# Performance work log

Hardware: AMD Instinct MI355X
Metric: run time of the kernel (lower is better)

The kernel has to match this reference:

```python
import jax, jax.numpy as jnp
import numpy as np

DPW = 1.0       # dist_push_weight
IW = 1.0        # intensity_weight
MINDIST = 0.05
MAXVAL = 255.0
KS = 11         # gaussian blur kernel size


def _gaussian_blur(img):
    """torchvision-style gaussian_blur with kernel_size=11, default sigma, reflect pad. img: [B,H,W]."""
    sigma = 0.3 * ((KS - 1) * 0.5 - 1) + 0.8  # = 2.0
    half = (KS - 1) * 0.5
    x = jnp.linspace(-half, half, KS)
    pdf = jnp.exp(-0.5 * (x / sigma) ** 2)
    k1 = (pdf / pdf.sum()).astype(img.dtype)
    pad = KS // 2
    xp = jnp.pad(img, ((0, 0), (pad, pad), (pad, pad)), mode='reflect')
    lhs = xp[:, None]  # [B,1,H+2p,W+2p]
    kh = k1.reshape(1, 1, KS, 1)
    kw = k1.reshape(1, 1, 1, KS)
    y = jax.lax.conv_general_dilated(lhs, kh, (1, 1), 'VALID')
    y = jax.lax.conv_general_dilated(y, kw, (1, 1), 'VALID')
    return y[:, 0]


def _dist_push(tr):
    """tr: [N,2]. mean over upper-triangle pairs of clamp(mindist - dist, 0)."""
    n = tr.shape[0]
    sq = jnp.sum(tr * tr, axis=-1)                       # [N]
    d2 = sq[:, None] + sq[None, :] - 2.0 * (tr @ tr.T)   # [N,N]
    d2 = jnp.maximum(d2, 0.0)
    mask = jnp.triu(jnp.ones((n, n), dtype=bool), k=1)
    d = jnp.sqrt(jnp.where(mask, d2, 1.0))               # safe sqrt off-mask
    vals = jnp.where(mask, jnp.maximum(MINDIST - d, 0.0), 0.0)
    npairs = n * (n - 1) // 2
    return jnp.sum(vals) / npairs


def _intensity(x, trace):
    """x: [H,W] blurred image, trace: [N,2] in [0,1]. Returns per-point bilinear-ish intensity [N]."""
    H, W = x.shape
    idx0 = trace[:, 0] * H
    idx1 = trace[:, 1] * W
    xp = jnp.pad(x, ((0, 2), (0, 2)), mode='reflect')    # reflect pad right/bottom by 2
    i0 = jax.lax.stop_gradient(jnp.floor(idx0 + 0.5))
    i1 = i0 + 1.0
    j0 = jax.lax.stop_gradient(jnp.floor(idx1 + 0.5))
    j1 = j0 + 1.0
    i0i = i0.astype(jnp.int32); i1i = i1.astype(jnp.int32)
    j0i = j0.astype(jnp.int32); j1i = j1.astype(jnp.int32)
    y00 = xp[i0i, j0i]
    y10 = xp[i1i, j0i]
    y01 = xp[i0i, j1i]
    out_ax0 = (i1 - idx0) * y00 + (idx0 - i0) * y10
    out_ax1 = (j1 - idx1) * y00 + (idx1 - j0) * y01
    return (out_ax0 + out_ax1) / 2.0


def setup_inputs() -> dict:
    key = jax.random.key(0)
    k1, k2 = jax.random.split(key)
    trace = jax.random.uniform(k1, (8, 4096, 2), dtype=jnp.float32)
    img = jax.random.uniform(k2, (8, 512, 512), dtype=jnp.float32)
    return {"trace": trace, "img": img}


def reference(trace, img):
    dist_push_loss = jnp.mean(jax.vmap(_dist_push)(trace))
    imgf = _gaussian_blur(img)
    intensity = jax.vmap(_intensity)(imgf, trace)   # [B,N]
    int_loss = jnp.mean(MAXVAL - intensity)
    return dist_push_loss * DPW + int_loss * IW
```

## Files before the change

kernel.cpp:

```cpp
#include <hip/hip_runtime.h>

#define IMW 512
#define NP 4096

#define GATHER_BLOCKS 128
#define DIST_BLOCKS 1024
#define TOTAL_BLOCKS (GATHER_BLOCKS + DIST_BLOCKS)

__device__ constexpr float KW[11] = {
    0.00881223f, 0.02714359f, 0.06511407f, 0.12164908f, 0.17699836f,
    0.20056542f, 0.17699836f, 0.12164908f, 0.06511407f, 0.02714359f, 0.00881223f};

__device__ __forceinline__ int refl(int r) {
    r = r < 0 ? -r : r;
    return r > 511 ? 1022 - r : r;
}

__global__ __launch_bounds__(256)
void fused_compute(const float* __restrict__ trace, const float* __restrict__ img,
                   float* __restrict__ partials) {
    const int tid = threadIdx.x;
    const int bx = blockIdx.x;
    __shared__ float2 pj[512];
    __shared__ float red[4];
    float local;

    if (bx < GATHER_BLOCKS) {
        const int b = bx >> 4;
        const int p = (bx & 15) * 256 + tid;
        const float2 t2 = ((const float2*)trace)[b * NP + p];
        const float idx0 = t2.x * 512.f, idx1 = t2.y * 512.f;
        const float i0f = floorf(idx0 + 0.5f), j0f = floorf(idx1 + 0.5f);
        const float wi = idx0 - i0f, wj = idx1 - j0f;
        const int i0 = (int)i0f, j0 = (int)j0f;
        const int mi0 = refl(i0), mi1 = refl(i0 + 1);
        const int mj0 = refl(j0), mj1 = refl(j0 + 1);
        const int ilo = min(mi0, mi1), jlo = min(mj0, mj1);
        const bool sr = mi0 > mi1, sc = mj0 > mj1;
        const float* srcb = img + b * (IMW * IMW);

        float v0[12], v1[12];
        int R[12];
#pragma unroll
        for (int a = 0; a < 12; ++a) R[a] = refl(ilo - 5 + a) * IMW;
#pragma unroll
        for (int c = 0; c < 12; ++c) {
            const int cc = refl(jlo - 5 + c);
            const float* col = srcb + cc;
            float lo = 0.f, hi = 0.f;
#pragma unroll
            for (int a = 0; a < 12; ++a) {
                const float pv = col[R[a]];
                if (a < 11) lo = fmaf(KW[a], pv, lo);
                if (a > 0) hi = fmaf(KW[a - 1], pv, hi);
            }
            v0[c] = sr ? hi : lo;
            v1[c] = sr ? lo : hi;
        }
        float y00lo = 0.f, y00hi = 0.f, y10lo = 0.f, y10hi = 0.f;
#pragma unroll
        for (int c = 0; c < 11; ++c) {
            y00lo = fmaf(KW[c], v0[c], y00lo);
            y00hi = fmaf(KW[c], v0[c + 1], y00hi);
            y10lo = fmaf(KW[c], v1[c], y10lo);
            y10hi = fmaf(KW[c], v1[c + 1], y10hi);
        }
        const float y00 = sc ? y00hi : y00lo;
        const float y01 = sc ? y00lo : y00hi;
        const float y10 = sc ? y10hi : y10lo;
        local = 0.5f * ((1.f - wi) * y00 + wi * y10 + (1.f - wj) * y00 + wj * y01);
    } else {
        const int d = bx - GATHER_BLOCKS;
        const int b = d >> 7, ib = (d >> 3) & 15, jc = d & 7;
        const float2* tb = (const float2*)(trace + b * NP * 2);
        const float2 pi = tb[ib * 256 + tid];
        pj[tid] = tb[jc * 512 + tid];
        pj[tid + 256] = tb[jc * 512 + tid + 256];
        __syncthreads();
        float s = 0.f;
#pragma unroll 8
        for (int j = 0; j < 512; ++j) {
            const float dx = pi.x - pj[j].x;
            const float dy = pi.y - pj[j].y;
            const float d2 = fmaf(dx, dx, dy * dy);
            s += fminf(__builtin_amdgcn_sqrtf(d2), 0.05f);
        }
        local = s;
    }

    for (int o = 32; o; o >>= 1) local += __shfl_down(local, o, 64);
    if ((tid & 63) == 0) red[tid >> 6] = local;
    __syncthreads();
    if (tid == 0) partials[bx] = red[0] + red[1] + red[2] + red[3];
}

__global__ __launch_bounds__(256)
void finalize(const float* __restrict__ partials, float* __restrict__ out) {
    const int tid = threadIdx.x;
    float sg = 0.f, sd = 0.f;
    for (int i = tid; i < TOTAL_BLOCKS; i += 256) {
        const float v = partials[i];
        if (i < GATHER_BLOCKS) sg += v; else sd += v;
    }
    for (int o = 32; o; o >>= 1) {
        sg += __shfl_down(sg, o, 64);
        sd += __shfl_down(sd, o, 64);
    }
    __shared__ float rg[4], rd[4];
    if ((tid & 63) == 0) { rg[tid >> 6] = sg; rd[tid >> 6] = sd; }
    __syncthreads();
    if (tid == 0) {
        const double M  = (double)(rd[0] + rd[1] + rd[2] + rd[3]);
        const double S1 = (double)(rg[0] + rg[1] + rg[2] + rg[3]);
        const double dp = (6709248.0 - M) / 134184960.0;
        const double il = 255.0 - S1 / 32768.0;
        out[0] = (float)(dp + il);
    }
}

extern "C" void kernel_launch(void* const* d_in, const int* in_sizes, int n_in,
                              void* d_out, int out_size, void* d_ws, size_t ws_size,
                              hipStream_t stream) {
    const float* trace = (const float*)d_in[0];
    const float* img = (const float*)d_in[1];
    float* partials = (float*)d_ws;
    float* out = (float*)d_out;

    fused_compute<<<TOTAL_BLOCKS, 256, 0, stream>>>(trace, img, partials);
    finalize<<<1, 256, 0, stream>>>(partials, out);
}
```

Baseline: 106.6 us.

## Replace all-pairs distance loop with per-batch uniform grid neighbor search

The pairwise dist-push term is now computed with a 20x20 uniform grid: each of 8 blocks bins its batch's 4096 points by counting sort in shared memory, then each point only tests the points in its 3x3 neighbouring cells against the 0.05 cutoff. This removes the O(N^2) dense distance evaluation. The gather path switches to row-major separable blur order, and both paths now use 1024-thread blocks, which cuts the grid from 1152 blocks to 40. The risks are low parallelism on a large GPU (only 8 distance blocks), serial prefix scans and atomics, and divergent per-thread loop lengths.

```diff
diff --git a/kernel.cpp b/kernel.cpp
--- a/kernel.cpp
+++ b/kernel.cpp
@@ -2,10 +2,14 @@
 
 #define IMW 512
 #define NP 4096
+#define NB 8
 
-#define GATHER_BLOCKS 128
-#define DIST_BLOCKS 1024
+#define GATHER_BLOCKS 32
+#define DIST_BLOCKS 8
 #define TOTAL_BLOCKS (GATHER_BLOCKS + DIST_BLOCKS)
+
+#define NCELL 20
+#define NCELL2 400
 
 __device__ constexpr float KW[11] = {
     0.00881223f, 0.02714359f, 0.06511407f, 0.12164908f, 0.17699836f,
@@ -16,19 +20,23 @@
     return r > 511 ? 1022 - r : r;
 }
 
-__global__ __launch_bounds__(256)
+__global__ __launch_bounds__(1024)
 void fused_compute(const float* __restrict__ trace, const float* __restrict__ img,
                    float* __restrict__ partials) {
     const int tid = threadIdx.x;
     const int bx = blockIdx.x;
-    __shared__ float2 pj[512];
-    __shared__ float red[4];
+    __shared__ float2 sorted[NP];
+    __shared__ int cellcnt[NCELL2];
+    __shared__ int cellstart[NCELL2];
+    __shared__ int cursor[NCELL2];
+    __shared__ int offs[512];
+    __shared__ float red[16];
     float local;
 
     if (bx < GATHER_BLOCKS) {
-        const int b = bx >> 4;
-        const int p = (bx & 15) * 256 + tid;
-        const float2 t2 = ((const float2*)trace)[b * NP + p];
+        const int p = bx * 1024 + tid;
+        const int b = p >> 12;
+        const float2 t2 = ((const float2*)trace)[b * NP + (p & (NP - 1))];
         const float idx0 = t2.x * 512.f, idx1 = t2.y * 512.f;
         const float i0f = floorf(idx0 + 0.5f), j0f = floorf(idx1 + 0.5f);
         const float wi = idx0 - i0f, wj = idx1 - j0f;
@@ -39,51 +47,91 @@
         const bool sr = mi0 > mi1, sc = mj0 > mj1;
         const float* srcb = img + b * (IMW * IMW);
 
-        float v0[12], v1[12];
-        int R[12];
+        int cc[12], R[12];
 #pragma unroll
-        for (int a = 0; a < 12; ++a) R[a] = refl(ilo - 5 + a) * IMW;
+        for (int c = 0; c < 12; ++c) cc[c] = refl(jlo - 5 + c);
 #pragma unroll
-        for (int c = 0; c < 12; ++c) {
-            const int cc = refl(jlo - 5 + c);
-            const float* col = srcb + cc;
+        for (int r = 0; r < 12; ++r) R[r] = refl(ilo - 5 + r) * IMW;
+
+        float A_lo = 0.f, A_hi = 0.f, B_lo = 0.f, B_hi = 0.f;
+#pragma unroll
+        for (int r = 0; r < 12; ++r) {
+            const float* base = srcb + R[r];
             float lo = 0.f, hi = 0.f;
 #pragma unroll
-            for (int a = 0; a < 12; ++a) {
-                const float pv = col[R[a]];
-                if (a < 11) lo = fmaf(KW[a], pv, lo);
-                if (a > 0) hi = fmaf(KW[a - 1], pv, hi);
+            for (int c = 0; c < 12; ++c) {
+                const float v = base[cc[c]];
+                if (c < 11) lo = fmaf(KW[c], v, lo);
+                if (c > 0) hi = fmaf(KW[c - 1], v, hi);
             }
-            v0[c] = sr ? hi : lo;
-            v1[c] = sr ? lo : hi;
+            if (r < 11) { A_lo = fmaf(KW[r], lo, A_lo); B_lo = fmaf(KW[r], hi, B_lo); }
+            if (r > 0)  { A_hi = fmaf(KW[r - 1], lo, A_hi); B_hi = fmaf(KW[r - 1], hi, B_hi); }
         }
-        float y00lo = 0.f, y00hi = 0.f, y10lo = 0.f, y10hi = 0.f;
-#pragma unroll
-        for (int c = 0; c < 11; ++c) {
-            y00lo = fmaf(KW[c], v0[c], y00lo);
-            y00hi = fmaf(KW[c], v0[c + 1], y00hi);
-            y10lo = fmaf(KW[c], v1[c], y10lo);
-            y10hi = fmaf(KW[c], v1[c + 1], y10hi);
-        }
-        const float y00 = sc ? y00hi : y00lo;
-        const float y01 = sc ? y00lo : y00hi;
-        const float y10 = sc ? y10hi : y10lo;
+        const float yA  = sr ? A_hi : A_lo;
+        const float yA1 = sr ? A_lo : A_hi;
+        const float yB  = sr ? B_hi : B_lo;
+        const float yB1 = sr ? B_lo : B_hi;
+        const float y00 = sc ? yB : yA;
+        const float y01 = sc ? yA : yB;
+        const float y10 = sc ? yB1 : yA1;
         local = 0.5f * ((1.f - wi) * y00 + wi * y10 + (1.f - wj) * y00 + wj * y01);
     } else {
-        const int d = bx - GATHER_BLOCKS;
-        const int b = d >> 7, ib = (d >> 3) & 15, jc = d & 7;
+        const int b = bx - GATHER_BLOCKS;
         const float2* tb = (const float2*)(trace + b * NP * 2);
-        const float2 pi = tb[ib * 256 + tid];
-        pj[tid] = tb[jc * 512 + tid];
-        pj[tid + 256] = tb[jc * 512 + tid + 256];
+        float2 r4[4];
+        int c4[4];
+#pragma unroll
+        for (int k = 0; k < 4; ++k) {
+            const float2 pt = tb[tid + 1024 * k];
+            r4[k] = pt;
+            const int cx = min((int)(pt.x * 20.f), NCELL - 1);
+            const int cy = min((int)(pt.y * 20.f), NCELL - 1);
+            c4[k] = cy * NCELL + cx;
+        }
+        if (tid < NCELL2) cellcnt[tid] = 0;
+        __syncthreads();
+#pragma unroll
+        for (int k = 0; k < 4; ++k) atomicAdd(&cellcnt[c4[k]], 1);
+        __syncthreads();
+        if (tid < 512) offs[tid] = (tid < NCELL2) ? cellcnt[tid] : 0;
+        __syncthreads();
+        for (int s = 1; s < 512; s <<= 1) {
+            int v = 0;
+            if (tid < 512 && tid >= s) v = offs[tid - s];
+            __syncthreads();
+            if (tid < 512) offs[tid] += v;
+            __syncthreads();
+        }
+        if (tid < NCELL2) {
+            const int st = offs[tid] - cellcnt[tid];
+            cellstart[tid] = st;
+            cursor[tid] = st;
+        }
+        __syncthreads();
+#pragma unroll
+        for (int k = 0; k < 4; ++k) {
+            const int pos = atomicAdd(&cursor[c4[k]], 1);
+            sorted[pos] = r4[k];
+        }
         __syncthreads();
         float s = 0.f;
-#pragma unroll 8
-        for (int j = 0; j < 512; ++j) {
-            const float dx = pi.x - pj[j].x;
-            const float dy = pi.y - pj[j].y;
-            const float d2 = fmaf(dx, dx, dy * dy);
-            s += fminf(__builtin_amdgcn_sqrtf(d2), 0.05f);
+#pragma unroll
+        for (int k = 0; k < 4; ++k) {
+            const float2 p = r4[k];
+            const int cy = c4[k] / NCELL, cx = c4[k] - cy * NCELL;
+            const int x0 = max(cx - 1, 0), x1 = min(cx + 1, NCELL - 1);
+            const int y0 = max(cy - 1, 0), y1 = min(cy + 1, NCELL - 1);
+            for (int ny = y0; ny <= y1; ++ny) {
+                const int rb = ny * NCELL;
+                int q = cellstart[rb + x0];
+                const int qe = cellstart[rb + x1] + cellcnt[rb + x1];
+                for (; q < qe; ++q) {
+                    const float2 o = sorted[q];
+                    const float dx = p.x - o.x, dy = p.y - o.y;
+                    const float d2 = fmaf(dx, dx, dy * dy);
+                    s += (d2 < 0.0025f) ? (0.05f - __builtin_amdgcn_sqrtf(d2)) : 0.f;
+                }
+            }
         }
         local = s;
     }
@@ -91,28 +139,30 @@
     for (int o = 32; o; o >>= 1) local += __shfl_down(local, o, 64);
     if ((tid & 63) == 0) red[tid >> 6] = local;
     __syncthreads();
-    if (tid == 0) partials[bx] = red[0] + red[1] + red[2] + red[3];
+    if (tid == 0) {
+        float t = 0.f;
+#pragma unroll
+        for (int w = 0; w < 16; ++w) t += red[w];
+        partials[bx] = t;
+    }
 }
 
-__global__ __launch_bounds__(256)
+__global__ __launch_bounds__(64)
 void finalize(const float* __restrict__ partials, float* __restrict__ out) {
     const int tid = threadIdx.x;
     float sg = 0.f, sd = 0.f;
-    for (int i = tid; i < TOTAL_BLOCKS; i += 256) {
-        const float v = partials[i];
-        if (i < GATHER_BLOCKS) sg += v; else sd += v;
+    if (tid < TOTAL_BLOCKS) {
+        const float v = partials[tid];
+        if (tid < GATHER_BLOCKS) sg = v; else sd = v;
     }
     for (int o = 32; o; o >>= 1) {
         sg += __shfl_down(sg, o, 64);
         sd += __shfl_down(sd, o, 64);
     }
-    __shared__ float rg[4], rd[4];
-    if ((tid & 63) == 0) { rg[tid >> 6] = sg; rd[tid >> 6] = sd; }
-    __syncthreads();
     if (tid == 0) {
-        const double M  = (double)(rd[0] + rd[1] + rd[2] + rd[3]);
-        const double S1 = (double)(rg[0] + rg[1] + rg[2] + rg[3]);
-        const double dp = (6709248.0 - M) / 134184960.0;
+        const double Sd = (double)sd;
+        const double S1 = (double)sg;
+        const double dp = (Sd - 1638.4) / 134184960.0;
         const double il = 255.0 - S1 / 32768.0;
         out[0] = (float)(dp + il);
     }
@@ -126,6 +176,6 @@
     float* partials = (float*)d_ws;
     float* out = (float*)d_out;
 
-    fused_compute<<<TOTAL_BLOCKS, 256, 0, stream>>>(trace, img, partials);
-    finalize<<<1, 256, 0, stream>>>(partials, out);
+    fused_compute<<<TOTAL_BLOCKS, 1024, 0, stream>>>(trace, img, partials);
+    finalize<<<1, 64, 0, stream>>>(partials, out);
 }
```

New measurement: 156.6 us. 1.47x slower.

## Replace all-pairs distance push with spatial row binning and split blur gather

Applied to the files above, without the earlier changes.

Points are binned by y coordinate into 20 strips, each 0.05 wide, matching the push cutoff. Each block compacts the points in its strip and the two neighbouring strips into shared memory with ballot-based stream compaction. It then only evaluates pairs within that band, where the cutoff distance guarantees no contribution is lost. Ordered pairs and self-pairs are counted and corrected in finalize. Separately, each intensity point's 12x12 blur footprint is now split across two lanes by row halves and combined with a shuffle, doubling gather parallelism. The costs are data-dependent load imbalance across strips and a larger shared-memory footprint that may limit occupancy.

```diff
diff --git a/kernel.cpp b/kernel.cpp
--- a/kernel.cpp
+++ b/kernel.cpp
@@ -3,9 +3,11 @@
 #define IMW 512
 #define NP 4096
 
-#define GATHER_BLOCKS 128
-#define DIST_BLOCKS 1024
-#define TOTAL_BLOCKS (GATHER_BLOCKS + DIST_BLOCKS)
+#define NROW 20
+#define DIST_BLOCKS 160
+#define GATHER_BLOCKS 256
+#define TOTAL_BLOCKS (DIST_BLOCKS + GATHER_BLOCKS)
+#define BS 256
 
 __device__ constexpr float KW[11] = {
     0.00881223f, 0.02714359f, 0.06511407f, 0.12164908f, 0.17699836f,
@@ -16,19 +18,65 @@
     return r > 511 ? 1022 - r : r;
 }
 
-__global__ __launch_bounds__(256)
+__global__ __launch_bounds__(BS)
 void fused_compute(const float* __restrict__ trace, const float* __restrict__ img,
                    float* __restrict__ partials) {
     const int tid = threadIdx.x;
     const int bx = blockIdx.x;
-    __shared__ float2 pj[512];
-    __shared__ float red[4];
+    const int lane = tid & 63;
+
+    __shared__ __align__(16) char smem[49184];
+    float2* band = (float2*)smem;
+    int* cidx = (int*)(smem + 32768);
+    int* cnts = (int*)(smem + 49152);
+    float* red = (float*)(smem + 49160);
+
     float local;
 
-    if (bx < GATHER_BLOCKS) {
-        const int b = bx >> 4;
-        const int p = (bx & 15) * 256 + tid;
-        const float2 t2 = ((const float2*)trace)[b * NP + p];
+    if (bx < DIST_BLOCKS) {
+        const int b = bx / NROW, row = bx - b * NROW;
+        const float2* tb = (const float2*)(trace + b * NP * 2);
+        if (tid == 0) { cnts[0] = 0; cnts[1] = 0; }
+        __syncthreads();
+        for (int k = tid; k < NP; k += BS) {
+            const float2 pt = tb[k];
+            const int cy = min((int)(pt.y * 20.f), NROW - 1);
+            const bool inb = (cy >= row - 1) && (cy <= row + 1);
+            const bool isc = (cy == row);
+            const unsigned long long mb = __ballot(inb);
+            const unsigned long long pre = mb & ((1ull << lane) - 1ull);
+            int base = 0;
+            if (lane == 0) base = atomicAdd(&cnts[0], __popcll(mb));
+            base = __shfl(base, 0, 64);
+            const int pos = base + __popcll(pre);
+            if (inb) band[pos] = pt;
+            const unsigned long long mc = __ballot(isc);
+            int cbase = 0;
+            if (lane == 0) cbase = atomicAdd(&cnts[1], __popcll(mc));
+            cbase = __shfl(cbase, 0, 64);
+            if (isc) cidx[cbase + __popcll(mc & ((1ull << lane) - 1ull))] = pos;
+        }
+        __syncthreads();
+        const int nb = cnts[0], nc = cnts[1];
+        float s = 0.f;
+        for (int c = tid; c < nc; c += BS) {
+            const float2 p = band[cidx[c]];
+            float acc = 0.f;
+            for (int q = 0; q < nb; ++q) {
+                const float2 o = band[q];
+                const float dx = p.x - o.x, dy = p.y - o.y;
+                const float d2 = fmaf(dx, dx, dy * dy);
+                acc += (d2 < 0.0025f) ? (0.05f - __builtin_amdgcn_sqrtf(d2)) : 0.f;
+            }
+            s += acc;
+        }
+        local = s;
+    } else {
+        const int g = bx - DIST_BLOCKS;
+        const int half = tid & 1;
+        const int p = g * 128 + (tid >> 1);
+        const int b = p >> 12;
+        const float2 t2 = ((const float2*)trace)[b * NP + (p & (NP - 1))];
         const float idx0 = t2.x * 512.f, idx1 = t2.y * 512.f;
         const float i0f = floorf(idx0 + 0.5f), j0f = floorf(idx1 + 0.5f);
         const float wi = idx0 - i0f, wj = idx1 - j0f;
@@ -39,56 +87,46 @@
         const bool sr = mi0 > mi1, sc = mj0 > mj1;
         const float* srcb = img + b * (IMW * IMW);
 
-        float v0[12], v1[12];
-        int R[12];
+        int cc[12];
 #pragma unroll
-        for (int a = 0; a < 12; ++a) R[a] = refl(ilo - 5 + a) * IMW;
+        for (int c = 0; c < 12; ++c) cc[c] = refl(jlo - 5 + c);
+
+        float A_lo = 0.f, A_hi = 0.f, B_lo = 0.f, B_hi = 0.f;
 #pragma unroll
-        for (int c = 0; c < 12; ++c) {
-            const int cc = refl(jlo - 5 + c);
-            const float* col = srcb + cc;
+        for (int rr = 0; rr < 6; ++rr) {
+            const int r = half ? rr + 6 : rr;
+            const float* base = srcb + refl(ilo - 5 + r) * IMW;
             float lo = 0.f, hi = 0.f;
 #pragma unroll
-            for (int a = 0; a < 12; ++a) {
-                const float pv = col[R[a]];
-                if (a < 11) lo = fmaf(KW[a], pv, lo);
-                if (a > 0) hi = fmaf(KW[a - 1], pv, hi);
+            for (int c = 0; c < 12; ++c) {
+                const float v = base[cc[c]];
+                if (c < 11) lo = fmaf(KW[c], v, lo);
+                if (c > 0) hi = fmaf(KW[c - 1], v, hi);
             }
-            v0[c] = sr ? hi : lo;
-            v1[c] = sr ? lo : hi;
+            const float wlo = half ? (rr < 5 ? KW[rr + 6] : 0.f) : KW[rr];
+            const float whi = half ? KW[rr + 5] : (rr > 0 ? KW[rr - 1] : 0.f);
+            A_lo = fmaf(wlo, lo, A_lo);
+            A_hi = fmaf(whi, lo, A_hi);
+            B_lo = fmaf(wlo, hi, B_lo);
+            B_hi = fmaf(whi, hi, B_hi);
         }
-        float y00lo = 0.f, y00hi = 0.f, y10lo = 0.f, y10hi = 0.f;
-#pragma unroll
-        for (int c = 0; c < 11; ++c) {
-            y00lo = fmaf(KW[c], v0[c], y00lo);
-            y00hi = fmaf(KW[c], v0[c + 1], y00hi);
-            y10lo = fmaf(KW[c], v1[c], y10lo);
-            y10hi = fmaf(KW[c], v1[c + 1], y10hi);
-        }
-        const float y00 = sc ? y00hi : y00lo;
-        const float y01 = sc ? y00lo : y00hi;
-        const float y10 = sc ? y10hi : y10lo;
-        local = 0.5f * ((1.f - wi) * y00 + wi * y10 + (1.f - wj) * y00 + wj * y01);
-    } else {
-        const int d = bx - GATHER_BLOCKS;
-        const int b = d >> 7, ib = (d >> 3) & 15, jc = d & 7;
-        const float2* tb = (const float2*)(trace + b * NP * 2);
-        const float2 pi = tb[ib * 256 + tid];
-        pj[tid] = tb[jc * 512 + tid];
-        pj[tid + 256] = tb[jc * 512 + tid + 256];
-        __syncthreads();
-        float s = 0.f;
-#pragma unroll 8
-        for (int j = 0; j < 512; ++j) {
-            const float dx = pi.x - pj[j].x;
-            const float dy = pi.y - pj[j].y;
-            const float d2 = fmaf(dx, dx, dy * dy);
-            s += fminf(__builtin_amdgcn_sqrtf(d2), 0.05f);
-        }
-        local = s;
+        A_lo += __shfl_xor(A_lo, 1, 64);
+        A_hi += __shfl_xor(A_hi, 1, 64);
+        B_lo += __shfl_xor(B_lo, 1, 64);
+        B_hi += __shfl_xor(B_hi, 1, 64);
+        const float yA  = sr ? A_hi : A_lo;
+        const float yA1 = sr ? A_lo : A_hi;
+        const float yB  = sr ? B_hi : B_lo;
+        const float yB1 = sr ? B_lo : B_hi;
+        const float y00 = sc ? yB : yA;
+        const float y01 = sc ? yA : yB;
+        const float y10 = sc ? yB1 : yA1;
+        const float inten = 0.5f * ((1.f - wi) * y00 + wi * y10 + (1.f - wj) * y00 + wj * y01);
+        local = (half == 0) ? inten : 0.f;
     }
 
     for (int o = 32; o; o >>= 1) local += __shfl_down(local, o, 64);
+    __syncthreads();
     if ((tid & 63) == 0) red[tid >> 6] = local;
     __syncthreads();
     if (tid == 0) partials[bx] = red[0] + red[1] + red[2] + red[3];
@@ -100,7 +138,7 @@
     float sg = 0.f, sd = 0.f;
     for (int i = tid; i < TOTAL_BLOCKS; i += 256) {
         const float v = partials[i];
-        if (i < GATHER_BLOCKS) sg += v; else sd += v;
+        if (i < DIST_BLOCKS) sd += v; else sg += v;
     }
     for (int o = 32; o; o >>= 1) {
         sg += __shfl_down(sg, o, 64);
@@ -110,9 +148,9 @@
     if ((tid & 63) == 0) { rg[tid >> 6] = sg; rd[tid >> 6] = sd; }
     __syncthreads();
     if (tid == 0) {
-        const double M  = (double)(rd[0] + rd[1] + rd[2] + rd[3]);
+        const double Sd = (double)(rd[0] + rd[1] + rd[2] + rd[3]);
         const double S1 = (double)(rg[0] + rg[1] + rg[2] + rg[3]);
-        const double dp = (6709248.0 - M) / 134184960.0;
+        const double dp = (Sd - 1638.4) / 134184960.0;
         const double il = 255.0 - S1 / 32768.0;
         out[0] = (float)(dp + il);
     }
@@ -126,6 +164,6 @@
     float* partials = (float*)d_ws;
     float* out = (float*)d_out;
 
-    fused_compute<<<TOTAL_BLOCKS, 256, 0, stream>>>(trace, img, partials);
+    fused_compute<<<TOTAL_BLOCKS, BS, 0, stream>>>(trace, img, partials);
     finalize<<<1, 256, 0, stream>>>(partials, out);
 }
```

After: 94.76 us. 11.1% less time.
